# Kernel tuning notes

Measured on AMD Instinct MI355X. Metric: run time of the kernel, lower is better.

## Reference

```python
import jax, jax.numpy as jnp
import numpy as np

B, L, D = 2, 4096, 768
H, HD = 12, 64
EPS = 1e-6


def setup_inputs() -> dict:
    key = jax.random.key(0)
    ks = jax.random.split(key, 5)
    x = jax.random.normal(ks[0], (B, L, D), dtype=jnp.float32)
    # realistic rope tables
    inv_freq = 1.0 / (10000.0 ** (np.arange(0, HD, 2, dtype=np.float32) / HD))
    t = np.arange(L, dtype=np.float32)
    freqs = np.outer(t, inv_freq)  # (L, HD/2)
    emb = np.concatenate([freqs, freqs], axis=-1)  # (L, HD)
    rope_cos = jnp.asarray(np.cos(emb))
    rope_sin = jnp.asarray(np.sin(emb))
    Wqkv = jax.random.normal(ks[1], (3 * D, D), dtype=jnp.float32) * (1.0 / np.sqrt(D))
    Wout = jax.random.normal(ks[2], (D, D), dtype=jnp.float32) * (1.0 / np.sqrt(D))
    q_norm_w = jnp.ones((HD,), dtype=jnp.float32)
    k_norm_w = jnp.ones((HD,), dtype=jnp.float32)
    return {"x": x, "rope_cos": rope_cos, "rope_sin": rope_sin,
            "Wqkv": Wqkv, "Wout": Wout,
            "q_norm_w": q_norm_w, "k_norm_w": k_norm_w}


def _rms_norm(x, w):
    # x: (..., HD); computed in float32 like the torch module
    norm = jax.lax.rsqrt(jnp.mean(jnp.square(x.astype(jnp.float32)), axis=-1, keepdims=True) + EPS)
    return (x.astype(jnp.float32) * norm).astype(x.dtype) * w


def _rotate_half(x):
    x1, x2 = jnp.split(x, 2, axis=-1)
    return jnp.concatenate([-x2, x1], axis=-1)


def reference(x, rope_cos, rope_sin, Wqkv, Wout, q_norm_w, k_norm_w):
    b, l, d = x.shape
    # fused QKV projection (Linear with no bias): x @ Wqkv.T
    qkv = jnp.einsum('bld,ed->ble', x, Wqkv).reshape(b, l, 3, H, HD)
    q, k, v = qkv[:, :, 0], qkv[:, :, 1], qkv[:, :, 2]  # (B, L, H, HD)
    q = jnp.transpose(q, (0, 2, 1, 3))  # (B, H, L, HD)
    k = jnp.transpose(k, (0, 2, 1, 3))
    v = jnp.transpose(v, (0, 2, 1, 3))
    # per-head RMSNorm on q and k
    q = _rms_norm(q, q_norm_w)
    k = _rms_norm(k, k_norm_w)
    # RoPE: cos/sin (L, HD) broadcast over (B, H)
    cos = rope_cos[None, None, :, :]
    sin = rope_sin[None, None, :, :]
    q = q * cos + _rotate_half(q) * sin
    k = k * cos + _rotate_half(k) * sin
    # scaled dot product attention (no mask)
    scale = 1.0 / jnp.sqrt(jnp.asarray(HD, dtype=q.dtype))
    scores = jnp.einsum('bhqd,bhkd->bhqk', q, k) * scale  # (B, H, L, L)
    attn = jax.nn.softmax(scores, axis=-1)
    out = jnp.einsum('bhqk,bhkd->bhqd', attn, v)  # (B, H, L, HD)
    out = jnp.transpose(out, (0, 2, 1, 3)).reshape(b, l, d)
    return jnp.einsum('bld,ed->ble', out, Wout)
```

## Files before the change

### kernel.cpp

```cpp
#include <hip/hip_runtime.h>
#include <hip/hip_bf16.h>

typedef float f32x4 __attribute__((ext_vector_type(4)));
typedef float f32x16 __attribute__((ext_vector_type(16)));
typedef short bf16x8 __attribute__((ext_vector_type(8)));
typedef unsigned short ushort8_t __attribute__((ext_vector_type(8)));

#define L_SEQ 4096
#define DMODEL 768
#define NHEAD 12
#define HDIM 64
#define QSCALE (0.125f * 1.44269504f)

__device__ __forceinline__ unsigned short f2bf(float f) {
    __hip_bfloat16 h = __float2bfloat16(f);
    return *reinterpret_cast<unsigned short*>(&h);
}

__device__ __forceinline__ unsigned pack2bf(float a, float b) {
    return (unsigned)f2bf(a) | ((unsigned)f2bf(b) << 16);
}

__device__ __forceinline__ void gload16(const void* g, void* l) {
    __builtin_amdgcn_global_load_lds(
        (const __attribute__((address_space(1))) unsigned int*)g,
        (__attribute__((address_space(3))) unsigned int*)l, 16, 0, 0);
}

__global__ __launch_bounds__(256) void cvt3_f32_bf16(
    const float* __restrict__ a, unsigned short* __restrict__ oa, int na,
    const float* __restrict__ bsrc, unsigned short* __restrict__ ob, int nb,
    const float* __restrict__ csrc, unsigned short* __restrict__ oc, int nc)
{
    int i = (blockIdx.x * 256 + threadIdx.x) * 4;
    const float* in; unsigned short* out;
    if (i < na) { in = a; out = oa; }
    else if (i < na + nb) { in = bsrc; out = ob; i -= na; }
    else if (i < na + nb + nc) { in = csrc; out = oc; i -= na + nb; }
    else return;
    float4 v = *reinterpret_cast<const float4*>(in + i);
    ushort4 o;
    o.x = f2bf(v.x); o.y = f2bf(v.y); o.z = f2bf(v.z); o.w = f2bf(v.w);
    *reinterpret_cast<ushort4*>(out + i) = o;
}

#define BM 128
#define BN 128
#define BKK 64

__global__ __launch_bounds__(256) void gemm_qkv_fused(
    const unsigned short* __restrict__ A, const unsigned short* __restrict__ Bt,
    const float* __restrict__ cosb, const float* __restrict__ sinb,
    const float* __restrict__ qw, const float* __restrict__ kw,
    unsigned short* __restrict__ Qb, unsigned short* __restrict__ Kb,
    unsigned short* __restrict__ Vt)
{
    __shared__ union SM {
        struct { unsigned short As[BM][BKK]; unsigned short Bs[BN][BKK]; } st;
        unsigned short ep[4][64][72];
    } sm;

    const int K = DMODEL;
    const int tid  = threadIdx.x;
    const int lane = tid & 63;
    const int wid  = tid >> 6;
    const int r = lane & 15, g = lane >> 4;
    const int wr = wid >> 1, wc = wid & 1;
    const int m0 = blockIdx.y * BM;
    const int n0 = blockIdx.x * BN;

    f32x4 acc[4][4];
    for (int i = 0; i < 4; ++i)
        for (int j = 0; j < 4; ++j)
            acc[i][j] = (f32x4){0.f, 0.f, 0.f, 0.f};

    for (int kt = 0; kt < K; kt += BKK) {
        __syncthreads();
        for (int p = 0; p < 4; ++p) {
            int idx = wid * 64 + p * 256 + lane;
            int row = idx >> 3;
            int ch  = (idx & 7) * 8;
            gload16(&A[(size_t)(m0 + row) * K + kt + ch],
                    (char*)sm.st.As + (size_t)(wid * 64 + p * 256) * 16);
            gload16(&Bt[(size_t)(n0 + row) * K + kt + ch],
                    (char*)sm.st.Bs + (size_t)(wid * 64 + p * 256) * 16);
        }
        __syncthreads();
        for (int k0 = 0; k0 < BKK; k0 += 32) {
            bf16x8 a[4], b[4];
            for (int i = 0; i < 4; ++i)
                a[i] = *reinterpret_cast<const bf16x8*>(&sm.st.As[wr * 64 + i * 16 + r][k0 + 8 * g]);
            for (int j = 0; j < 4; ++j)
                b[j] = *reinterpret_cast<const bf16x8*>(&sm.st.Bs[wc * 64 + j * 16 + r][k0 + 8 * g]);
            for (int i = 0; i < 4; ++i)
                for (int j = 0; j < 4; ++j)
                    acc[i][j] = __builtin_amdgcn_mfma_f32_16x16x32_bf16(a[i], b[j], acc[i][j], 0, 0, 0);
        }
    }

    __syncthreads();

    const int e0  = n0 + wc * 64;
    const int sec = e0 / DMODEL;
    const int h   = (e0 % DMODEL) / HDIM;
    const int row0 = m0 + wr * 64;
    const int b   = row0 >> 12;
    const int l0  = row0 & (L_SEQ - 1);
    unsigned short (*ep)[72] = sm.ep[wid];

    if (sec < 2) {
        const float* nw = (sec == 0) ? qw : kw;
        float wv[4];
        for (int j = 0; j < 4; ++j) wv[j] = nw[j * 16 + r];
        for (int i = 0; i < 4; ++i) {
            for (int t = 0; t < 4; ++t) {
                float ss = acc[i][0][t] * acc[i][0][t] + acc[i][1][t] * acc[i][1][t]
                         + acc[i][2][t] * acc[i][2][t] + acc[i][3][t] * acc[i][3][t];
                ss += __shfl_xor(ss, 1);
                ss += __shfl_xor(ss, 2);
                ss += __shfl_xor(ss, 4);
                ss += __shfl_xor(ss, 8);
                float inv = rsqrtf(ss * (1.f / 64.f) + 1e-6f);
                int lr = i * 16 + 4 * g + t;
                int l  = l0 + lr;
                float qn[4];
                for (int j = 0; j < 4; ++j) qn[j] = acc[i][j][t] * inv * wv[j];
                for (int j = 0; j < 4; ++j) {
                    int d = j * 16 + r;
                    float c = cosb[l * HDIM + d], s = sinb[l * HDIM + d];
                    float sgn = (j < 2) ? -1.f : 1.f;
                    float res = qn[j] * c + sgn * qn[j ^ 2] * s;
                    if (sec == 0) res *= QSCALE;
                    ep[lr][d] = f2bf(res);
                }
            }
        }
        unsigned short* dst = ((sec == 0) ? Qb : Kb)
            + ((size_t)(b * NHEAD + h) * L_SEQ + l0) * HDIM;
        for (int it = 0; it < 8; ++it) {
            int idx = it * 64 + lane;
            int lr = idx >> 3, ch = (idx & 7) * 8;
            ushort8_t v = *reinterpret_cast<const ushort8_t*>(&ep[lr][ch]);
            *reinterpret_cast<ushort8_t*>(&dst[(size_t)lr * HDIM + ch]) = v;
        }
    } else {
        for (int i = 0; i < 4; ++i)
            for (int t = 0; t < 4; ++t) {
                int lr = i * 16 + 4 * g + t;
                for (int j = 0; j < 4; ++j)
                    ep[j * 16 + r][lr] = f2bf(acc[i][j][t]);
            }
        unsigned short* dst = Vt + ((size_t)(b * NHEAD + h) * HDIM) * L_SEQ + l0;
        for (int it = 0; it < 8; ++it) {
            int idx = it * 64 + lane;
            int d = idx >> 3, ch = (idx & 7) * 8;
            ushort8_t v = *reinterpret_cast<const ushort8_t*>(&ep[d][ch]);
            *reinterpret_cast<ushort8_t*>(&dst[(size_t)d * L_SEQ + ch]) = v;
        }
    }
}

__global__ __launch_bounds__(256) void gemm_bf16_nt(
    const unsigned short* __restrict__ A, const unsigned short* __restrict__ Bt,
    float* __restrict__ C, int M, int N, int K)
{
    __shared__ unsigned short As[BM][BKK];
    __shared__ unsigned short Bs[BN][BKK];
    const int tid  = threadIdx.x;
    const int lane = tid & 63;
    const int wid  = tid >> 6;
    const int r = lane & 15, g = lane >> 4;
    const int wr = wid >> 1, wc = wid & 1;
    const int m0 = blockIdx.y * BM;
    const int n0 = blockIdx.x * BN;

    f32x4 acc[4][4];
    for (int i = 0; i < 4; ++i)
        for (int j = 0; j < 4; ++j)
            acc[i][j] = (f32x4){0.f, 0.f, 0.f, 0.f};

    for (int kt = 0; kt < K; kt += BKK) {
        __syncthreads();
        for (int p = 0; p < 4; ++p) {
            int idx = wid * 64 + p * 256 + lane;
            int row = idx >> 3;
            int ch  = (idx & 7) * 8;
            gload16(&A[(size_t)(m0 + row) * K + kt + ch],
                    (char*)As + (size_t)(wid * 64 + p * 256) * 16);
            gload16(&Bt[(size_t)(n0 + row) * K + kt + ch],
                    (char*)Bs + (size_t)(wid * 64 + p * 256) * 16);
        }
        __syncthreads();
        for (int k0 = 0; k0 < BKK; k0 += 32) {
            bf16x8 a[4], b[4];
            for (int i = 0; i < 4; ++i)
                a[i] = *reinterpret_cast<const bf16x8*>(&As[wr * 64 + i * 16 + r][k0 + 8 * g]);
            for (int j = 0; j < 4; ++j)
                b[j] = *reinterpret_cast<const bf16x8*>(&Bs[wc * 64 + j * 16 + r][k0 + 8 * g]);
            for (int i = 0; i < 4; ++i)
                for (int j = 0; j < 4; ++j)
                    acc[i][j] = __builtin_amdgcn_mfma_f32_16x16x32_bf16(a[i], b[j], acc[i][j], 0, 0, 0);
        }
    }
    for (int i = 0; i < 4; ++i)
        for (int j = 0; j < 4; ++j)
            for (int t = 0; t < 4; ++t) {
                int row = m0 + wr * 64 + i * 16 + 4 * g + t;
                int col = n0 + wc * 64 + j * 16 + r;
                C[(size_t)row * N + col] = acc[i][j][t];
            }
}

__global__ __launch_bounds__(256, 3) void flashattn(
    const unsigned short* __restrict__ Qb, const unsigned short* __restrict__ Kb,
    const unsigned short* __restrict__ Vt, unsigned short* __restrict__ aob)
{
    __shared__ unsigned short Ks[2][64 * 64];
    __shared__ unsigned short Vs[2][64 * 64];

    const int lin = blockIdx.x;
    const int bh = (lin & 7) + 8 * (lin >> 8);
    const int qblk = (lin >> 3) & 31;
    const int b = bh / NHEAD, h = bh % NHEAD;
    const int tid = threadIdx.x;
    const int wid = tid >> 6, lane = tid & 63;
    const int l31 = lane & 31, half = lane >> 5;
    const int q0 = qblk * 128 + wid * 32;

    bf16x8 qf[4];
    {
        const unsigned short* Qp = Qb + ((size_t)bh * L_SEQ + q0 + l31) * HDIM + 8 * half;
        for (int dt = 0; dt < 4; ++dt)
            qf[dt] = *reinterpret_cast<const bf16x8*>(Qp + dt * 16);
    }

    bf16x8 onesf;
    for (int e = 0; e < 8; ++e) onesf[e] = (l31 == 0) ? (short)0x3F80 : (short)0;

    const unsigned short* Kbase = Kb + (size_t)bh * L_SEQ * HDIM;
    const unsigned short* Vbase = Vt + (size_t)bh * HDIM * L_SEQ;

    f32x16 o0 = {0.f}, o1 = {0.f}, o_l = {0.f};
    for (int e = 0; e < 16; ++e) { o0[e] = 0.f; o1[e] = 0.f; o_l[e] = 0.f; }

    auto stage = [&](int buf, int kb) {
        for (int p = 0; p < 2; ++p) {
            int idx = wid * 64 + p * 256 + lane;
            int row = idx >> 3;
            int colb = ((idx & 7) * 16) ^ ((row & 7) << 4);
            gload16(Kbase + (size_t)(kb + row) * HDIM + (colb >> 1),
                    (char*)Ks[buf] + (size_t)(wid * 64 + p * 256) * 16);
            gload16(Vbase + (size_t)row * L_SEQ + kb + (colb >> 1),
                    (char*)Vs[buf] + (size_t)(wid * 64 + p * 256) * 16);
        }
    };

    stage(0, 0);
    __syncthreads();
    int cur = 0;

    for (int kb = 0; kb < L_SEQ; kb += 64) {
        if (kb + 64 < L_SEQ) stage(cur ^ 1, kb + 64);
        const char* KsB = (const char*)Ks[cur];
        const char* VsB = (const char*)Vs[cur];

        f32x16 s0 = o_l, s1 = o_l;
        for (int e = 0; e < 16; ++e) { s0[e] = 0.f; s1[e] = 0.f; }
        __builtin_amdgcn_s_setprio(1);
        for (int kh = 0; kh < 2; ++kh) {
            int krow = kh * 32 + l31;
            const char* rowp = KsB + krow * 128;
            int sw = (krow & 7) << 4;
            f32x16& s = kh ? s1 : s0;
            for (int dt = 0; dt < 4; ++dt) {
                bf16x8 kf = *reinterpret_cast<const bf16x8*>(rowp + ((dt * 32 + half * 16) ^ sw));
                s = __builtin_amdgcn_mfma_f32_32x32x16_bf16(kf, qf[dt], s, 0, 0, 0);
            }
        }
        __builtin_amdgcn_s_setprio(0);

        bf16x8 pa[4];
        for (int kh = 0; kh < 2; ++kh) {
            const f32x16& s = kh ? s1 : s0;
            float p[16];
            for (int e = 0; e < 16; ++e) p[e] = __builtin_amdgcn_exp2f(s[e]);
            for (int kk = 0; kk < 2; ++kk) {
                unsigned A = pack2bf(p[8 * kk + 0], p[8 * kk + 1]);
                unsigned Bp = pack2bf(p[8 * kk + 2], p[8 * kk + 3]);
                unsigned C = pack2bf(p[8 * kk + 4], p[8 * kk + 5]);
                unsigned D = pack2bf(p[8 * kk + 6], p[8 * kk + 7]);
                asm volatile("v_permlane32_swap_b32 %0, %1" : "+v"(A), "+v"(C));
                asm volatile("v_permlane32_swap_b32 %0, %1" : "+v"(Bp), "+v"(D));
                union { unsigned u[4]; bf16x8 v; } t;
                t.u[0] = A; t.u[1] = Bp; t.u[2] = C; t.u[3] = D;
                pa[2 * kh + kk] = t.v;
            }
        }

        __builtin_amdgcn_s_setprio(1);
        for (int kt = 0; kt < 4; ++kt)
            o_l = __builtin_amdgcn_mfma_f32_32x32x16_bf16(pa[kt], onesf, o_l, 0, 0, 0);
        for (int dh = 0; dh < 2; ++dh) {
            int drow = dh * 32 + l31;
            const char* rowp = VsB + drow * 128;
            int sw = (drow & 7) << 4;
            f32x16& o = dh ? o1 : o0;
            for (int kt = 0; kt < 4; ++kt) {
                bf16x8 vf = *reinterpret_cast<const bf16x8*>(rowp + ((kt * 32 + half * 16) ^ sw));
                o = __builtin_amdgcn_mfma_f32_32x32x16_bf16(pa[kt], vf, o, 0, 0, 0);
            }
        }
        __builtin_amdgcn_s_setprio(0);
        __syncthreads();
        cur ^= 1;
    }

    float linv[16];
    for (int j = 0; j < 16; ++j)
        linv[j] = 1.f / __shfl(o_l[j], lane & 32);
    for (int j = 0; j < 16; ++j) {
        int q = (j & 3) + 8 * (j >> 2) + 4 * half;
        size_t base = ((size_t)(b * L_SEQ + q0 + q)) * DMODEL + h * HDIM + l31;
        aob[base] = f2bf(o0[j] * linv[j]);
        aob[base + 32] = f2bf(o1[j] * linv[j]);
    }
}

extern "C" void kernel_launch(void* const* d_in, const int* in_sizes, int n_in,
                              void* d_out, int out_size, void* d_ws, size_t ws_size,
                              hipStream_t stream) {
    const float* x        = (const float*)d_in[0];
    const float* rope_cos = (const float*)d_in[1];
    const float* rope_sin = (const float*)d_in[2];
    const float* Wqkv     = (const float*)d_in[3];
    const float* Wout     = (const float*)d_in[4];
    const float* q_norm_w = (const float*)d_in[5];
    const float* k_norm_w = (const float*)d_in[6];
    float* out = (float*)d_out;

    const int BL = 2 * L_SEQ;
    const int nx    = BL * DMODEL;
    const int nwqkv = 3 * DMODEL * DMODEL;
    const int nwout = DMODEL * DMODEL;

    char* w = (char*)d_ws;
    unsigned short* xb    = (unsigned short*)w; w += (size_t)nx * 2;
    unsigned short* wqkvb = (unsigned short*)w; w += (size_t)nwqkv * 2;
    unsigned short* woutb = (unsigned short*)w; w += (size_t)nwout * 2;
    unsigned short* Qb    = (unsigned short*)w; w += (size_t)nx * 2;
    unsigned short* Kb    = (unsigned short*)w; w += (size_t)nx * 2;
    unsigned short* Vtb   = (unsigned short*)w; w += (size_t)nx * 2;
    unsigned short* aob   = (unsigned short*)w; w += (size_t)nx * 2;

    {
        int total = (nx + nwqkv + nwout) / 4;
        cvt3_f32_bf16<<<(total + 255) / 256, 256, 0, stream>>>(
            x, xb, nx, Wqkv, wqkvb, nwqkv, Wout, woutb, nwout);
    }

    {
        dim3 grid(3 * DMODEL / BN, BL / BM);
        gemm_qkv_fused<<<grid, 256, 0, stream>>>(xb, wqkvb, rope_cos, rope_sin,
                                                 q_norm_w, k_norm_w, Qb, Kb, Vtb);
    }

    flashattn<<<768, 256, 0, stream>>>(Qb, Kb, Vtb, aob);

    {
        dim3 grid(DMODEL / BN, BL / BM);
        gemm_bf16_nt<<<grid, 256, 0, stream>>>(aob, woutb, out, BL, DMODEL, DMODEL);
    }
}
```

Before: 230.9 us.

## Software-pipeline flash attention so QK of next tile overlaps softmax and PV

Restructures the attention loop into a two-stage software pipeline. K and V staging are split and offset by one tile, so the QK^T MFMAs for tile t+1 are issued alongside the exp/pack and PV MFMAs for tile t. Global-load addresses are precomputed once per thread. Inline asm is made non-volatile so the compiler can schedule it. This is meant to hide exp latency and LDS loads behind matrix work, at the cost of more live accumulator registers (four extra f32x16), which may hurt occupancy at launch_bounds 3.

```diff
diff --git a/kernel.cpp b/kernel.cpp
--- a/kernel.cpp
+++ b/kernel.cpp
@@ -215,8 +215,8 @@
     const unsigned short* __restrict__ Qb, const unsigned short* __restrict__ Kb,
     const unsigned short* __restrict__ Vt, unsigned short* __restrict__ aob)
 {
-    __shared__ unsigned short Ks[2][64 * 64];
-    __shared__ unsigned short Vs[2][64 * 64];
+    __shared__ unsigned short Ksm[2][64 * 64];
+    __shared__ unsigned short Vsm[2][64 * 64];
 
     const int lin = blockIdx.x;
     const int bh = (lin & 7) + 8 * (lin >> 8);
@@ -240,48 +240,48 @@
     const unsigned short* Kbase = Kb + (size_t)bh * L_SEQ * HDIM;
     const unsigned short* Vbase = Vt + (size_t)bh * HDIM * L_SEQ;
 
-    f32x16 o0 = {0.f}, o1 = {0.f}, o_l = {0.f};
-    for (int e = 0; e < 16; ++e) { o0[e] = 0.f; o1[e] = 0.f; o_l[e] = 0.f; }
-
-    auto stage = [&](int buf, int kb) {
-        for (int p = 0; p < 2; ++p) {
-            int idx = wid * 64 + p * 256 + lane;
-            int row = idx >> 3;
-            int colb = ((idx & 7) * 16) ^ ((row & 7) << 4);
-            gload16(Kbase + (size_t)(kb + row) * HDIM + (colb >> 1),
-                    (char*)Ks[buf] + (size_t)(wid * 64 + p * 256) * 16);
-            gload16(Vbase + (size_t)row * L_SEQ + kb + (colb >> 1),
-                    (char*)Vs[buf] + (size_t)(wid * 64 + p * 256) * 16);
-        }
+    const int idx0 = tid, idx1 = tid + 256;
+    const int row0 = idx0 >> 3, row1 = idx1 >> 3;
+    const int c0 = ((idx0 & 7) * 16) ^ ((row0 & 7) << 4);
+    const int c1 = ((idx1 & 7) * 16) ^ ((row1 & 7) << 4);
+    const char* kp0 = (const char*)(Kbase + (size_t)row0 * HDIM) + c0;
+    const char* kp1 = (const char*)(Kbase + (size_t)row1 * HDIM) + c1;
+    const char* vp0 = (const char*)(Vbase + (size_t)row0 * L_SEQ) + c0;
+    const char* vp1 = (const char*)(Vbase + (size_t)row1 * L_SEQ) + c1;
+
+    f32x16 o0, o1, o_l, sA0, sA1, sB0, sB1;
+    for (int e = 0; e < 16; ++e) {
+        o0[e] = 0.f; o1[e] = 0.f; o_l[e] = 0.f;
+        sA0[e] = 0.f; sA1[e] = 0.f; sB0[e] = 0.f; sB1[e] = 0.f;
+    }
+
+    auto stageK = [&](int buf, int t) {
+        size_t off = (size_t)t * (64 * HDIM * 2);
+        gload16(kp0 + off, (char*)Ksm[buf] + wid * 1024);
+        gload16(kp1 + off, (char*)Ksm[buf] + wid * 1024 + 4096);
     };
-
-    stage(0, 0);
-    __syncthreads();
-    int cur = 0;
-
-    for (int kb = 0; kb < L_SEQ; kb += 64) {
-        if (kb + 64 < L_SEQ) stage(cur ^ 1, kb + 64);
-        const char* KsB = (const char*)Ks[cur];
-        const char* VsB = (const char*)Vs[cur];
-
-        f32x16 s0 = o_l, s1 = o_l;
-        for (int e = 0; e < 16; ++e) { s0[e] = 0.f; s1[e] = 0.f; }
-        __builtin_amdgcn_s_setprio(1);
+    auto stageV = [&](int buf, int t) {
+        size_t off = (size_t)t * 128;
+        gload16(vp0 + off, (char*)Vsm[buf] + wid * 1024);
+        gload16(vp1 + off, (char*)Vsm[buf] + wid * 1024 + 4096);
+    };
+
+    auto qk = [&](f32x16& s0, f32x16& s1, const unsigned short* Kbuf) {
+        const char* rp0 = (const char*)Kbuf + l31 * 128;
+        const char* rp1 = rp0 + 32 * 128;
+        const int sw = (l31 & 7) << 4;
+        for (int dt = 0; dt < 4; ++dt) {
+            int co = (dt * 32 + half * 16) ^ sw;
+            bf16x8 kf0 = *reinterpret_cast<const bf16x8*>(rp0 + co);
+            bf16x8 kf1 = *reinterpret_cast<const bf16x8*>(rp1 + co);
+            s0 = __builtin_amdgcn_mfma_f32_32x32x16_bf16(kf0, qf[dt], s0, 0, 0, 0);
+            s1 = __builtin_amdgcn_mfma_f32_32x32x16_bf16(kf1, qf[dt], s1, 0, 0, 0);
+        }
+    };
+
+    auto softmax_pa = [&](f32x16& s0, f32x16& s1, bf16x8* pa) {
         for (int kh = 0; kh < 2; ++kh) {
-            int krow = kh * 32 + l31;
-            const char* rowp = KsB + krow * 128;
-            int sw = (krow & 7) << 4;
             f32x16& s = kh ? s1 : s0;
-            for (int dt = 0; dt < 4; ++dt) {
-                bf16x8 kf = *reinterpret_cast<const bf16x8*>(rowp + ((dt * 32 + half * 16) ^ sw));
-                s = __builtin_amdgcn_mfma_f32_32x32x16_bf16(kf, qf[dt], s, 0, 0, 0);
-            }
-        }
-        __builtin_amdgcn_s_setprio(0);
-
-        bf16x8 pa[4];
-        for (int kh = 0; kh < 2; ++kh) {
-            const f32x16& s = kh ? s1 : s0;
             float p[16];
             for (int e = 0; e < 16; ++e) p[e] = __builtin_amdgcn_exp2f(s[e]);
             for (int kk = 0; kk < 2; ++kk) {
@@ -289,31 +289,67 @@
                 unsigned Bp = pack2bf(p[8 * kk + 2], p[8 * kk + 3]);
                 unsigned C = pack2bf(p[8 * kk + 4], p[8 * kk + 5]);
                 unsigned D = pack2bf(p[8 * kk + 6], p[8 * kk + 7]);
-                asm volatile("v_permlane32_swap_b32 %0, %1" : "+v"(A), "+v"(C));
-                asm volatile("v_permlane32_swap_b32 %0, %1" : "+v"(Bp), "+v"(D));
-                union { unsigned u[4]; bf16x8 v; } t;
-                t.u[0] = A; t.u[1] = Bp; t.u[2] = C; t.u[3] = D;
-                pa[2 * kh + kk] = t.v;
+                asm("v_permlane32_swap_b32 %0, %1" : "+v"(A), "+v"(C));
+                asm("v_permlane32_swap_b32 %0, %1" : "+v"(Bp), "+v"(D));
+                union { unsigned u[4]; bf16x8 v; } tt;
+                tt.u[0] = A; tt.u[1] = Bp; tt.u[2] = C; tt.u[3] = D;
+                pa[2 * kh + kk] = tt.v;
             }
-        }
-
-        __builtin_amdgcn_s_setprio(1);
+            for (int e = 0; e < 16; ++e) s[e] = 0.f;
+        }
+    };
+
+    auto pv = [&](const bf16x8* pa, const unsigned short* Vbuf) {
         for (int kt = 0; kt < 4; ++kt)
             o_l = __builtin_amdgcn_mfma_f32_32x32x16_bf16(pa[kt], onesf, o_l, 0, 0, 0);
-        for (int dh = 0; dh < 2; ++dh) {
-            int drow = dh * 32 + l31;
-            const char* rowp = VsB + drow * 128;
-            int sw = (drow & 7) << 4;
-            f32x16& o = dh ? o1 : o0;
-            for (int kt = 0; kt < 4; ++kt) {
-                bf16x8 vf = *reinterpret_cast<const bf16x8*>(rowp + ((kt * 32 + half * 16) ^ sw));
-                o = __builtin_amdgcn_mfma_f32_32x32x16_bf16(pa[kt], vf, o, 0, 0, 0);
-            }
-        }
+        const char* rp0 = (const char*)Vbuf + l31 * 128;
+        const char* rp1 = rp0 + 32 * 128;
+        const int sw = (l31 & 7) << 4;
+        for (int kt = 0; kt < 4; ++kt) {
+            int co = (kt * 32 + half * 16) ^ sw;
+            bf16x8 vf0 = *reinterpret_cast<const bf16x8*>(rp0 + co);
+            bf16x8 vf1 = *reinterpret_cast<const bf16x8*>(rp1 + co);
+            o0 = __builtin_amdgcn_mfma_f32_32x32x16_bf16(pa[kt], vf0, o0, 0, 0, 0);
+            o1 = __builtin_amdgcn_mfma_f32_32x32x16_bf16(pa[kt], vf1, o1, 0, 0, 0);
+        }
+    };
+
+    stageK(0, 0);
+    __syncthreads();
+    stageK(1, 1); stageV(0, 0);
+    __builtin_amdgcn_s_setprio(1);
+    qk(sA0, sA1, Ksm[0]);
+    __builtin_amdgcn_s_setprio(0);
+    __syncthreads();
+
+    bf16x8 pa[4];
+    for (int i = 0; i < 31; ++i) {
+        int t1 = 2 * i + 1;
+        stageK(0, t1 + 1); stageV(1, t1);
+        __builtin_amdgcn_s_setprio(1);
+        qk(sB0, sB1, Ksm[1]);
+        softmax_pa(sA0, sA1, pa);
+        pv(pa, Vsm[0]);
         __builtin_amdgcn_s_setprio(0);
         __syncthreads();
-        cur ^= 1;
-    }
+        int t2 = t1 + 1;
+        stageK(1, t2 + 1); stageV(0, t2);
+        __builtin_amdgcn_s_setprio(1);
+        qk(sA0, sA1, Ksm[0]);
+        softmax_pa(sB0, sB1, pa);
+        pv(pa, Vsm[1]);
+        __builtin_amdgcn_s_setprio(0);
+        __syncthreads();
+    }
+    stageV(1, 63);
+    __builtin_amdgcn_s_setprio(1);
+    qk(sB0, sB1, Ksm[1]);
+    softmax_pa(sA0, sA1, pa);
+    pv(pa, Vsm[0]);
+    __builtin_amdgcn_s_setprio(0);
+    __syncthreads();
+    softmax_pa(sB0, sB1, pa);
+    pv(pa, Vsm[1]);
 
     float linv[16];
     for (int j = 0; j < 16; ++j)
```

New measurement: 222.8 us. 1.04x faster.
